# Kernel optimization log

Measured on AMD Instinct MI355X. Metric: run time of the kernel, lower is better.

The kernel has to match this reference:

```python
import jax, jax.numpy as jnp
import numpy as np

LN_EPS = 1e-12


def _conv1d(x, w, b, pad):
    # x: (B, Cin, L), w: (Cout, Cin, K) -> (B, Cout, L)
    y = jax.lax.conv_general_dilated(x, w, window_strides=(1,), padding=[(pad, pad)],
                                     dimension_numbers=('NCH', 'OIH', 'NCH'))
    return y + b[None, :, None]


def setup_inputs() -> dict:
    key = jax.random.key(0)
    ks = jax.random.split(key, 6)
    B, L, C, KH = 4, 4096, 768, 7
    return {
        'hidden_states': jax.random.normal(ks[0], (B, L, C), jnp.float32),
        'attention_mask': jnp.ones((B, L), jnp.float32),
        'special_tokens_mask': jnp.zeros((B, L), jnp.float32),
        'ln_w': jnp.ones((C,), jnp.float32),
        'ln_b': jnp.zeros((C,), jnp.float32),
        'off_w': jax.random.normal(ks[1], (KH, C, KH), jnp.float32) * 0.02,
        'off_b': jnp.zeros((KH,), jnp.float32),
        'mod_w': jax.random.normal(ks[2], (KH, C, KH), jnp.float32) * 0.02,
        'mod_b': jnp.zeros((KH,), jnp.float32),
        'reg_w': jax.random.normal(ks[3], (C, C, KH), jnp.float32) * 0.02,
    }


def reference(hidden_states, attention_mask, special_tokens_mask,
              ln_w, ln_b, off_w, off_b, mod_w, mod_b, reg_w):
    B, L, C = hidden_states.shape
    kh = off_w.shape[0]
    pad = kh // 2
    residual = hidden_states

    # input layernorm (biased variance, like torch.nn.LayerNorm)
    mu = hidden_states.mean(-1, keepdims=True)
    var = hidden_states.var(-1, keepdims=True)
    h = (hidden_states - mu) * jax.lax.rsqrt(var + LN_EPS) * ln_w + ln_b

    ht = jnp.swapaxes(h, 1, 2)  # (B, C, L)
    off = _conv1d(ht, off_w, off_b, pad)                    # (B, kh, L) seq-axis offsets
    mod = 2.0 * jax.nn.sigmoid(_conv1d(ht, mod_w, mod_b, pad))  # (B, kh, L)

    # mask special tokens / padding before sampling
    gate = ((1.0 - special_tokens_mask) * attention_mask)[:, None, :]
    xm = ht * gate  # (B, C, L)

    # deformable 1D sampling positions: p - pad + k + off[b,k,p]
    base = (jnp.arange(L, dtype=jnp.float32) - pad)[None, :] + jnp.arange(kh, dtype=jnp.float32)[:, None]  # (kh, L)
    pos = base[None, :, :] + off  # (B, kh, L)
    f = jnp.floor(pos)
    t = pos - f                   # (B, kh, L) frac
    fi = f.astype(jnp.int32)

    def gather(idx):
        # linear-sample tap with zero padding outside [0, L-1]
        inb = ((idx >= 0) & (idx <= L - 1)).astype(xm.dtype)  # (B, kh, L)
        idxc = jnp.clip(idx, 0, L - 1)
        v = jax.vmap(lambda xb, ib: xb[:, ib])(xm, idxc)      # (B, C, kh, L)
        return v * inb[:, None, :, :]

    sample = gather(fi) * (1.0 - t)[:, None] + gather(fi + 1) * t[:, None]  # (B, C, kh, L)
    sample = sample * mod[:, None]  # modulated

    out = jnp.einsum('ock,bckp->bop', reg_w, sample)  # (B, C, L)
    out = jnp.swapaxes(out, 1, 2) + residual          # (B, L, C)
    return out
```

## Files before the change

### kernel.cpp

```cpp
#include <hip/hip_runtime.h>
#include <math.h>

#define BB 4
#define LL 4096
#define CC 768
#define KHH 7
#define PADK 3
#define ROWS (BB*LL)
#define NKP  (BB*KHH*LL)
#define GK   (KHH*CC)
#define NT   (GK/64)
#define NKC  (GK/8)

typedef unsigned short ushort8 __attribute__((ext_vector_type(8)));
typedef short short8 __attribute__((ext_vector_type(8)));
typedef float f32x4 __attribute__((ext_vector_type(4)));

__device__ __forceinline__ float bf2f(unsigned short u) {
    return __uint_as_float(((unsigned)u) << 16);
}
__device__ __forceinline__ unsigned short f2bf(float x) {
    unsigned u = __float_as_uint(x);
    return (unsigned short)((u + 0x7FFFu + ((u >> 16) & 1u)) >> 16);
}

__global__ __launch_bounds__(256) void k_ln(const float* __restrict__ x,
        const float* __restrict__ mask, const float* __restrict__ special,
        const float* __restrict__ lnw, const float* __restrict__ lnb,
        unsigned short* __restrict__ hb, float* __restrict__ gate) {
    int row = blockIdx.x;
    const float* xr = x + (size_t)row * CC;
    float s = 0.f, q = 0.f;
    for (int i = threadIdx.x; i < CC; i += 256) { float v = xr[i]; s += v; q += v * v; }
    for (int o = 32; o; o >>= 1) { s += __shfl_xor(s, o); q += __shfl_xor(q, o); }
    __shared__ float ss[4], sq[4];
    int wid = threadIdx.x >> 6;
    if ((threadIdx.x & 63) == 0) { ss[wid] = s; sq[wid] = q; }
    __syncthreads();
    s = ss[0] + ss[1] + ss[2] + ss[3];
    q = sq[0] + sq[1] + sq[2] + sq[3];
    float mu  = s * (1.f / CC);
    float var = fmaxf(q * (1.f / CC) - mu * mu, 0.f);
    float rstd = rsqrtf(var + 1e-12f);
    unsigned short* hr = hb + (size_t)row * CC;
    for (int i = threadIdx.x; i < CC; i += 256)
        hr[i] = f2bf((xr[i] - mu) * rstd * lnw[i] + lnb[i]);
    if (threadIdx.x == 0) gate[row] = (1.f - special[row]) * mask[row];
}

__global__ __launch_bounds__(256) void k_wbt(const float* __restrict__ rw,
                                             unsigned short* __restrict__ wbt) {
    __shared__ float s[GK];
    int o = blockIdx.x;
    for (int i = threadIdx.x; i < GK; i += 256) s[i] = rw[(size_t)o * GK + i];
    __syncthreads();
    for (int kc = threadIdx.x; kc < NKC; kc += 256) {
        int k = kc / 96;
        int c0 = (kc - k * 96) * 8;
        ushort8 r;
#pragma unroll
        for (int e = 0; e < 8; ++e) r[e] = f2bf(s[(c0 + e) * KHH + k]);
        *(ushort8*)(wbt + ((size_t)kc * CC + o) * 8) = r;
    }
}

__global__ __launch_bounds__(256) void k_wcb(const float* __restrict__ ow, const float* __restrict__ mw,
                                             unsigned short* __restrict__ wcb) {
    int i = blockIdx.x;
    for (int c = threadIdx.x; c < CC; c += 256) {
        float v = 0.f;
        if (i < 49)      v = ow[(size_t)(i / 7) * (CC * KHH) + (size_t)c * KHH + (i % 7)];
        else if (i < 98) { int j = i - 49; v = mw[(size_t)(j / 7) * (CC * KHH) + (size_t)c * KHH + (j % 7)]; }
        wcb[(size_t)i * CC + c] = f2bf(v);
    }
}

__global__ __launch_bounds__(256) void k_dg2(const unsigned short* __restrict__ A,
        const unsigned short* __restrict__ Bm, float* __restrict__ d) {
    __shared__ __align__(16) char As[128 * 128];
    __shared__ __align__(16) char Bs[128 * 128];
    int r0 = blockIdx.x * 128;
    int t = threadIdx.x;
    int lane = t & 63, w = t >> 6;
    int wr = w >> 1, wc = w & 1;
    f32x4 acc[4][4];
#pragma unroll
    for (int m = 0; m < 4; ++m)
#pragma unroll
        for (int n = 0; n < 4; ++n) acc[m][n] = (f32x4){0.f, 0.f, 0.f, 0.f};
    int lr = lane & 15;
    int lkb0 = (lane >> 4) * 16;
    for (int kk = 0; kk < CC; kk += 64) {
#pragma unroll
        for (int s = 0; s < 4; ++s) {
            int byteoff = (s * 256 + t) * 16;
            int row = byteoff >> 7;
            int colb = byteoff & 127;
            int sw = (row * 128 + colb) ^ ((row & 7) << 4);
            *(ushort8*)(As + sw) = *(const ushort8*)(A + (size_t)(r0 + row) * CC + kk + (colb >> 1));
            *(ushort8*)(Bs + sw) = *(const ushort8*)(Bm + (size_t)row * CC + kk + (colb >> 1));
        }
        __syncthreads();
#pragma unroll
        for (int ks = 0; ks < 2; ++ks) {
            short8 av[4], bv[4];
            int lkb = lkb0 + ks * 64;
#pragma unroll
            for (int m = 0; m < 4; ++m) {
                int ar = wr * 64 + m * 16 + lr;
                av[m] = *(const short8*)(As + ((ar * 128 + lkb) ^ ((ar & 7) << 4)));
            }
#pragma unroll
            for (int n = 0; n < 4; ++n) {
                int br = wc * 64 + n * 16 + lr;
                bv[n] = *(const short8*)(Bs + ((br * 128 + lkb) ^ ((br & 7) << 4)));
            }
#pragma unroll
            for (int m = 0; m < 4; ++m)
#pragma unroll
                for (int n = 0; n < 4; ++n)
                    acc[m][n] = __builtin_amdgcn_mfma_f32_16x16x32_bf16(av[m], bv[n], acc[m][n], 0, 0, 0);
        }
        __syncthreads();
    }
    int lr4 = (lane >> 4) * 4, lc = lane & 15;
#pragma unroll
    for (int m = 0; m < 4; ++m) {
        int gr = r0 + wr * 64 + m * 16 + lr4;
#pragma unroll
        for (int n = 0; n < 4; ++n) {
            int gc = wc * 64 + n * 16 + lc;
#pragma unroll
            for (int j = 0; j < 4; ++j)
                d[(size_t)(gr + j) * 128 + gc] = acc[m][n][j];
        }
    }
}

__global__ __launch_bounds__(256) void k_off(const float* __restrict__ d,
        const float* __restrict__ offb, const float* __restrict__ modb,
        const float* __restrict__ gate,
        int* __restrict__ idx0, int* __restrict__ idx1,
        float* __restrict__ w0a, float* __restrict__ w1a) {
    int flat = blockIdx.x * 256 + threadIdx.x;
    if (flat >= NKP) return;
    int p = flat & (LL - 1);
    int k = (flat >> 12) % KHH;
    int b = flat / (KHH * LL);
    float offa = offb[k], moda = modb[k];
#pragma unroll
    for (int j = 0; j < KHH; ++j) {
        int q = p + j - PADK;
        if (q >= 0 && q < LL) {
            const float* dr = d + (size_t)(b * LL + q) * 128;
            offa += dr[k * 7 + j];
            moda += dr[49 + k * 7 + j];
        }
    }
    float modv = 2.f / (1.f + expf(-moda));
    float pos = (float)(p - PADK + k) + offa;
    pos = fminf(fmaxf(pos, -1.0e9f), 1.0e9f);
    float f = floorf(pos);
    float tf = pos - f;
    int i0 = (int)f;
    int i1 = i0 + 1;
    float in0 = (i0 >= 0 && i0 < LL) ? 1.f : 0.f;
    float in1 = (i1 >= 0 && i1 < LL) ? 1.f : 0.f;
    int c0 = min(max(i0, 0), LL - 1);
    int c1 = min(max(i1, 0), LL - 1);
    float g0 = gate[b * LL + c0] * in0;
    float g1 = gate[b * LL + c1] * in1;
    w0a[flat] = modv * (1.f - tf) * g0;
    w1a[flat] = modv * tf * g1;
    idx0[flat] = c0;
    idx1[flat] = c1;
}


#define STEPOFF 49152
#define KSOFF   24576

#define LOADB(Q, KS, D0, D1, D2, D3, D4, D5) do { \
    const unsigned short* _q = (Q) + (KS) * KSOFF; \
    D0 = *(const short8*)(_q); \
    D1 = *(const short8*)(_q + 128); \
    D2 = *(const short8*)(_q + 256); \
    D3 = *(const short8*)(_q + 384); \
    D4 = *(const short8*)(_q + 512); \
    D5 = *(const short8*)(_q + 640); \
} while (0)

#define MFMA_ROW(AV, M, B0, B1, B2, B3, B4, B5) \
    acc[M][0] = __builtin_amdgcn_mfma_f32_16x16x32_bf16(AV, B0, acc[M][0], 0, 0, 0); \
    acc[M][1] = __builtin_amdgcn_mfma_f32_16x16x32_bf16(AV, B1, acc[M][1], 0, 0, 0); \
    acc[M][2] = __builtin_amdgcn_mfma_f32_16x16x32_bf16(AV, B2, acc[M][2], 0, 0, 0); \
    acc[M][3] = __builtin_amdgcn_mfma_f32_16x16x32_bf16(AV, B3, acc[M][3], 0, 0, 0); \
    acc[M][4] = __builtin_amdgcn_mfma_f32_16x16x32_bf16(AV, B4, acc[M][4], 0, 0, 0); \
    acc[M][5] = __builtin_amdgcn_mfma_f32_16x16x32_bf16(AV, B5, acc[M][5], 0, 0, 0);

#define COMPUTE_KS(ASB, KS, B0, B1, B2, B3, B4, B5) do { \
    __builtin_amdgcn_s_setprio(1); \
    int _lkb = ke0 * 2 + (KS) * 64; \
    short8 _av0, _av1, _av2, _av3; \
    { int ar = wr * 64 + 0 * 16 + lr; _av0 = *(const short8*)((ASB) + ar * 128 + (_lkb ^ ((ar & 7) << 4))); } \
    { int ar = wr * 64 + 1 * 16 + lr; _av1 = *(const short8*)((ASB) + ar * 128 + (_lkb ^ ((ar & 7) << 4))); } \
    { int ar = wr * 64 + 2 * 16 + lr; _av2 = *(const short8*)((ASB) + ar * 128 + (_lkb ^ ((ar & 7) << 4))); } \
    { int ar = wr * 64 + 3 * 16 + lr; _av3 = *(const short8*)((ASB) + ar * 128 + (_lkb ^ ((ar & 7) << 4))); } \
    MFMA_ROW(_av0, 0, B0, B1, B2, B3, B4, B5) \
    MFMA_ROW(_av1, 1, B0, B1, B2, B3, B4, B5) \
    MFMA_ROW(_av2, 2, B0, B1, B2, B3, B4, B5) \
    MFMA_ROW(_av3, 3, B0, B1, B2, B3, B4, B5) \
    __builtin_amdgcn_s_setprio(0); \
} while (0)

__global__ __launch_bounds__(512, 2) void k_fgemm(const unsigned short* __restrict__ hb,
        const unsigned short* __restrict__ Wbt,
        const int* __restrict__ idx0, const int* __restrict__ idx1,
        const float* __restrict__ w0a, const float* __restrict__ w1a,
        const float* __restrict__ resid, float* __restrict__ out) {
    __shared__ __align__(16) char As[2][128 * 128];

    int bid = blockIdx.x;
    int nhalf = (bid & 7) >> 2;
    int rowtile = (bid >> 3) * 4 + (bid & 3);
    int r0 = rowtile * 128;
    int o0 = nhalf * 384;
    int b = r0 >> 12;
    int p0 = r0 & (LL - 1);
    int pbase = ((b * KHH) << 12) + p0;
    const unsigned short* hbB = hb + (size_t)b * LL * CC;

    int t = threadIdx.x;
    int lane = t & 63, w = t >> 6;
    int wr = w >> 2, wc = w & 3;
    int lr = lane & 15;
    int ke0 = (lane >> 4) * 8;

    const unsigned short* pB = Wbt + ((size_t)(lane >> 4) * CC + o0 + wc * 96 + lr) * 8;

    int arow = t >> 2, aseg = t & 3;
    int acolb = aseg * 32;
    int aswz0 = arow * 128 + (acolb ^ ((arow & 7) << 4));
    int aswz1 = arow * 128 + ((acolb + 16) ^ ((arow & 7) << 4));

    f32x4 acc[4][6];
#pragma unroll
    for (int m = 0; m < 4; ++m)
#pragma unroll
        for (int n = 0; n < 6; ++n) acc[m][n] = (f32x4){0.f, 0.f, 0.f, 0.f};

    int g0 = 0, g1 = 0;
    float wa = 0.f, wbv = 0.f;
    int cur_tap = -1;

    ushort8 la0, la1, la2, la3;
    short8 S0_0, S0_1, S0_2, S0_3, S0_4, S0_5;
    short8 S1_0, S1_1, S1_2, S1_3, S1_4, S1_5;
    short8 S2_0, S2_1, S2_2, S2_3, S2_4, S2_5;

    auto loadA = [&](int tap, int c0) {
        if (tap != cur_tap) {
            int pf = pbase + (tap << 12) + arow;
            g0 = idx0[pf]; g1 = idx1[pf];
            wa = w0a[pf];  wbv = w1a[pf];
            cur_tap = tap;
        }
        const unsigned short* s0 = hbB + (size_t)g0 * CC + c0 + aseg * 16;
        const unsigned short* s1 = hbB + (size_t)g1 * CC + c0 + aseg * 16;
        la0 = *(const ushort8*)(s0);
        la1 = *(const ushort8*)(s0 + 8);
        la2 = *(const ushort8*)(s1);
        la3 = *(const ushort8*)(s1 + 8);
    };

    auto writeA = [&](char* Asb) {
        ushort8 ra, rb;
#pragma unroll
        for (int e = 0; e < 8; ++e) ra[e] = f2bf(fmaf(wa, bf2f(la0[e]), wbv * bf2f(la2[e])));
#pragma unroll
        for (int e = 0; e < 8; ++e) rb[e] = f2bf(fmaf(wa, bf2f(la1[e]), wbv * bf2f(la3[e])));
        *(ushort8*)(Asb + aswz0) = ra;
        *(ushort8*)(Asb + aswz1) = rb;
    };

    loadA(0, 0);
    LOADB(pB, 0, S0_0, S0_1, S0_2, S0_3, S0_4, S0_5);
    LOADB(pB, 1, S1_0, S1_1, S1_2, S1_3, S1_4, S1_5);
    writeA(As[0]);
    __syncthreads();

    int tap_c = 0, c0_c = 0;
    for (int sp = 0; sp < NT; sp += 2) {
        {
            int s = sp;
            int tap_n = tap_c, c0_n = c0_c + 64;
            if (c0_n == CC) { c0_n = 0; ++tap_n; }
            bool more = (s + 1 < NT);
            const unsigned short* pN = pB + STEPOFF;
            if (more) {
                LOADB(pN, 0, S2_0, S2_1, S2_2, S2_3, S2_4, S2_5);
                loadA(tap_n, c0_n);
            }
            __builtin_amdgcn_sched_barrier(0);
            COMPUTE_KS(As[0], 0, S0_0, S0_1, S0_2, S0_3, S0_4, S0_5);
            COMPUTE_KS(As[0], 1, S1_0, S1_1, S1_2, S1_3, S1_4, S1_5);
            __builtin_amdgcn_sched_barrier(0);
            if (more) {
                LOADB(pN, 1, S1_0, S1_1, S1_2, S1_3, S1_4, S1_5);
                writeA(As[1]);
            }
            __syncthreads();
            pB = pN;
            tap_c = tap_n; c0_c = c0_n;
        }
        {
            int s = sp + 1;
            if (s >= NT) break;
            int tap_n = tap_c, c0_n = c0_c + 64;
            if (c0_n == CC) { c0_n = 0; ++tap_n; }
            bool more = (s + 1 < NT);
            const unsigned short* pN = pB + STEPOFF;
            if (more) {
                LOADB(pN, 0, S0_0, S0_1, S0_2, S0_3, S0_4, S0_5);
                loadA(tap_n, c0_n);
            }
            __builtin_amdgcn_sched_barrier(0);
            COMPUTE_KS(As[1], 0, S2_0, S2_1, S2_2, S2_3, S2_4, S2_5);
            COMPUTE_KS(As[1], 1, S1_0, S1_1, S1_2, S1_3, S1_4, S1_5);
            __builtin_amdgcn_sched_barrier(0);
            if (more) {
                LOADB(pN, 1, S1_0, S1_1, S1_2, S1_3, S1_4, S1_5);
                writeA(As[0]);
            }
            __syncthreads();
            pB = pN;
            tap_c = tap_n; c0_c = c0_n;
        }
    }

    int lr4 = (lane >> 4) * 4, lc = lane & 15;
#pragma unroll
    for (int m = 0; m < 4; ++m) {
        int gr = r0 + wr * 64 + m * 16 + lr4;
#pragma unroll
        for (int n = 0; n < 6; ++n) {
            int gc = o0 + wc * 96 + n * 16 + lc;
#pragma unroll
            for (int j = 0; j < 4; ++j) {
                size_t idx = (size_t)(gr + j) * CC + gc;
                out[idx] = acc[m][n][j] + resid[idx];
            }
        }
    }
}

extern "C" void kernel_launch(void* const* d_in, const int* in_sizes, int n_in,
                              void* d_out, int out_size, void* d_ws, size_t ws_size,
                              hipStream_t stream) {
    const float* x   = (const float*)d_in[0];
    const float* am  = (const float*)d_in[1];
    const float* stm = (const float*)d_in[2];
    const float* lnw = (const float*)d_in[3];
    const float* lnb = (const float*)d_in[4];
    const float* ow  = (const float*)d_in[5];
    const float* ob  = (const float*)d_in[6];
    const float* mw  = (const float*)d_in[7];
    const float* mb  = (const float*)d_in[8];
    const float* rw  = (const float*)d_in[9];
    float* out = (float*)d_out;

    char* ws = (char*)d_ws;
    size_t off = 0;
    auto carve = [&](size_t bytes) -> char* {
        char* p = ws + off;
        off += (bytes + 255) & ~(size_t)255;
        return p;
    };
    unsigned short* hb  = (unsigned short*)carve((size_t)ROWS * CC * 2);
    unsigned short* wbt = (unsigned short*)carve((size_t)NKC * CC * 8 * 2);
    unsigned short* wcb = (unsigned short*)carve((size_t)128 * CC * 2);
    float* d    = (float*)carve((size_t)ROWS * 128 * 4);
    float* gate = (float*)carve((size_t)ROWS * 4);
    int*   i0   = (int*)carve((size_t)NKP * 4);
    int*   i1   = (int*)carve((size_t)NKP * 4);
    float* w0   = (float*)carve((size_t)NKP * 4);
    float* w1   = (float*)carve((size_t)NKP * 4);

    k_ln<<<ROWS, 256, 0, stream>>>(x, am, stm, lnw, lnb, hb, gate);
    k_wbt<<<CC, 256, 0, stream>>>(rw, wbt);
    k_wcb<<<128, 256, 0, stream>>>(ow, mw, wcb);
    k_dg2<<<ROWS / 128, 256, 0, stream>>>(hb, wcb, d);
    k_off<<<NKP / 256, 256, 0, stream>>>(d, ob, mb, gate, i0, i1, w0, w1);
    k_fgemm<<<256, 512, 0, stream>>>(hb, wbt, i0, i1, w0, w1, x, out);
}
```

Before: 210.3 us.

## Retile fused gather-GEMM to 128x192 tiles with 4 waves and 512 blocks

Changes the fused deformable-gather GEMM from 128x384 output tiles with 8 waves (2x4) to 128x192 tiles with 4 waves, each wave covering all 128 rows and 48 columns. The grid doubles to 512 blocks of 256 threads, and each thread now gathers and blends 32 channels per step instead of 16. The goal is more blocks per GPU for better load balance and occupancy, and less B-register pressure per wave. The cost is that each gathered A tile is reused across fewer output columns, so the gather and blend work is redone twice as often per output.

```diff
diff --git a/kernel.cpp b/kernel.cpp
--- a/kernel.cpp
+++ b/kernel.cpp
@@ -180,40 +180,42 @@
 #define STEPOFF 49152
 #define KSOFF   24576
 
-#define LOADB(Q, KS, D0, D1, D2, D3, D4, D5) do { \
+#define LOADB3(Q, KS, D0, D1, D2) do { \
     const unsigned short* _q = (Q) + (KS) * KSOFF; \
     D0 = *(const short8*)(_q); \
     D1 = *(const short8*)(_q + 128); \
     D2 = *(const short8*)(_q + 256); \
-    D3 = *(const short8*)(_q + 384); \
-    D4 = *(const short8*)(_q + 512); \
-    D5 = *(const short8*)(_q + 640); \
 } while (0)
 
-#define MFMA_ROW(AV, M, B0, B1, B2, B3, B4, B5) \
+#define MFMA_ROW3(AV, M, B0, B1, B2) \
     acc[M][0] = __builtin_amdgcn_mfma_f32_16x16x32_bf16(AV, B0, acc[M][0], 0, 0, 0); \
     acc[M][1] = __builtin_amdgcn_mfma_f32_16x16x32_bf16(AV, B1, acc[M][1], 0, 0, 0); \
-    acc[M][2] = __builtin_amdgcn_mfma_f32_16x16x32_bf16(AV, B2, acc[M][2], 0, 0, 0); \
-    acc[M][3] = __builtin_amdgcn_mfma_f32_16x16x32_bf16(AV, B3, acc[M][3], 0, 0, 0); \
-    acc[M][4] = __builtin_amdgcn_mfma_f32_16x16x32_bf16(AV, B4, acc[M][4], 0, 0, 0); \
-    acc[M][5] = __builtin_amdgcn_mfma_f32_16x16x32_bf16(AV, B5, acc[M][5], 0, 0, 0);
-
-#define COMPUTE_KS(ASB, KS, B0, B1, B2, B3, B4, B5) do { \
+    acc[M][2] = __builtin_amdgcn_mfma_f32_16x16x32_bf16(AV, B2, acc[M][2], 0, 0, 0);
+
+#define COMPUTE_KS3(ASB, KS, B0, B1, B2) do { \
     __builtin_amdgcn_s_setprio(1); \
     int _lkb = ke0 * 2 + (KS) * 64; \
-    short8 _av0, _av1, _av2, _av3; \
-    { int ar = wr * 64 + 0 * 16 + lr; _av0 = *(const short8*)((ASB) + ar * 128 + (_lkb ^ ((ar & 7) << 4))); } \
-    { int ar = wr * 64 + 1 * 16 + lr; _av1 = *(const short8*)((ASB) + ar * 128 + (_lkb ^ ((ar & 7) << 4))); } \
-    { int ar = wr * 64 + 2 * 16 + lr; _av2 = *(const short8*)((ASB) + ar * 128 + (_lkb ^ ((ar & 7) << 4))); } \
-    { int ar = wr * 64 + 3 * 16 + lr; _av3 = *(const short8*)((ASB) + ar * 128 + (_lkb ^ ((ar & 7) << 4))); } \
-    MFMA_ROW(_av0, 0, B0, B1, B2, B3, B4, B5) \
-    MFMA_ROW(_av1, 1, B0, B1, B2, B3, B4, B5) \
-    MFMA_ROW(_av2, 2, B0, B1, B2, B3, B4, B5) \
-    MFMA_ROW(_av3, 3, B0, B1, B2, B3, B4, B5) \
+    short8 _av0, _av1, _av2, _av3, _av4, _av5, _av6, _av7; \
+    { int ar = 0 * 16 + lr; _av0 = *(const short8*)((ASB) + ar * 128 + (_lkb ^ ((ar & 7) << 4))); } \
+    { int ar = 1 * 16 + lr; _av1 = *(const short8*)((ASB) + ar * 128 + (_lkb ^ ((ar & 7) << 4))); } \
+    { int ar = 2 * 16 + lr; _av2 = *(const short8*)((ASB) + ar * 128 + (_lkb ^ ((ar & 7) << 4))); } \
+    { int ar = 3 * 16 + lr; _av3 = *(const short8*)((ASB) + ar * 128 + (_lkb ^ ((ar & 7) << 4))); } \
+    MFMA_ROW3(_av0, 0, B0, B1, B2) \
+    MFMA_ROW3(_av1, 1, B0, B1, B2) \
+    MFMA_ROW3(_av2, 2, B0, B1, B2) \
+    MFMA_ROW3(_av3, 3, B0, B1, B2) \
+    { int ar = 4 * 16 + lr; _av4 = *(const short8*)((ASB) + ar * 128 + (_lkb ^ ((ar & 7) << 4))); } \
+    { int ar = 5 * 16 + lr; _av5 = *(const short8*)((ASB) + ar * 128 + (_lkb ^ ((ar & 7) << 4))); } \
+    { int ar = 6 * 16 + lr; _av6 = *(const short8*)((ASB) + ar * 128 + (_lkb ^ ((ar & 7) << 4))); } \
+    { int ar = 7 * 16 + lr; _av7 = *(const short8*)((ASB) + ar * 128 + (_lkb ^ ((ar & 7) << 4))); } \
+    MFMA_ROW3(_av4, 4, B0, B1, B2) \
+    MFMA_ROW3(_av5, 5, B0, B1, B2) \
+    MFMA_ROW3(_av6, 6, B0, B1, B2) \
+    MFMA_ROW3(_av7, 7, B0, B1, B2) \
     __builtin_amdgcn_s_setprio(0); \
 } while (0)
 
-__global__ __launch_bounds__(512, 2) void k_fgemm(const unsigned short* __restrict__ hb,
+__global__ __launch_bounds__(256, 2) void k_fgemm(const unsigned short* __restrict__ hb,
         const unsigned short* __restrict__ Wbt,
         const int* __restrict__ idx0, const int* __restrict__ idx1,
         const float* __restrict__ w0a, const float* __restrict__ w1a,
@@ -221,42 +223,44 @@
     __shared__ __align__(16) char As[2][128 * 128];
 
     int bid = blockIdx.x;
-    int nhalf = (bid & 7) >> 2;
-    int rowtile = (bid >> 3) * 4 + (bid & 3);
+    int nq = (bid & 7) >> 1;
+    int rowtile = (bid >> 3) * 2 + (bid & 1);
     int r0 = rowtile * 128;
-    int o0 = nhalf * 384;
+    int o0 = nq * 192;
     int b = r0 >> 12;
     int p0 = r0 & (LL - 1);
     int pbase = ((b * KHH) << 12) + p0;
     const unsigned short* hbB = hb + (size_t)b * LL * CC;
 
     int t = threadIdx.x;
-    int lane = t & 63, w = t >> 6;
-    int wr = w >> 2, wc = w & 3;
+    int lane = t & 63, wc = t >> 6;
     int lr = lane & 15;
     int ke0 = (lane >> 4) * 8;
 
-    const unsigned short* pB = Wbt + ((size_t)(lane >> 4) * CC + o0 + wc * 96 + lr) * 8;
-
-    int arow = t >> 2, aseg = t & 3;
-    int acolb = aseg * 32;
-    int aswz0 = arow * 128 + (acolb ^ ((arow & 7) << 4));
-    int aswz1 = arow * 128 + ((acolb + 16) ^ ((arow & 7) << 4));
-
-    f32x4 acc[4][6];
-#pragma unroll
-    for (int m = 0; m < 4; ++m)
-#pragma unroll
-        for (int n = 0; n < 6; ++n) acc[m][n] = (f32x4){0.f, 0.f, 0.f, 0.f};
+    const unsigned short* pB = Wbt + ((size_t)(lane >> 4) * CC + o0 + wc * 48 + lr) * 8;
+
+    int arow = t >> 1, aseg = t & 1;
+    int abase = arow * 128;
+    int axor = (arow & 7) << 4;
+    int asw0 = abase + ((aseg * 64 +  0) ^ axor);
+    int asw1 = abase + ((aseg * 64 + 16) ^ axor);
+    int asw2 = abase + ((aseg * 64 + 32) ^ axor);
+    int asw3 = abase + ((aseg * 64 + 48) ^ axor);
+
+    f32x4 acc[8][3];
+#pragma unroll
+    for (int m = 0; m < 8; ++m)
+#pragma unroll
+        for (int n = 0; n < 3; ++n) acc[m][n] = (f32x4){0.f, 0.f, 0.f, 0.f};
 
     int g0 = 0, g1 = 0;
     float wa = 0.f, wbv = 0.f;
     int cur_tap = -1;
 
-    ushort8 la0, la1, la2, la3;
-    short8 S0_0, S0_1, S0_2, S0_3, S0_4, S0_5;
-    short8 S1_0, S1_1, S1_2, S1_3, S1_4, S1_5;
-    short8 S2_0, S2_1, S2_2, S2_3, S2_4, S2_5;
+    ushort8 la0, la1, la2, la3, la4, la5, la6, la7;
+    short8 S0_0, S0_1, S0_2;
+    short8 S1_0, S1_1, S1_2;
+    short8 S2_0, S2_1, S2_2;
 
     auto loadA = [&](int tap, int c0) {
         if (tap != cur_tap) {
@@ -265,48 +269,57 @@
             wa = w0a[pf];  wbv = w1a[pf];
             cur_tap = tap;
         }
-        const unsigned short* s0 = hbB + (size_t)g0 * CC + c0 + aseg * 16;
-        const unsigned short* s1 = hbB + (size_t)g1 * CC + c0 + aseg * 16;
+        const unsigned short* s0 = hbB + (size_t)g0 * CC + c0 + aseg * 32;
+        const unsigned short* s1 = hbB + (size_t)g1 * CC + c0 + aseg * 32;
         la0 = *(const ushort8*)(s0);
         la1 = *(const ushort8*)(s0 + 8);
-        la2 = *(const ushort8*)(s1);
-        la3 = *(const ushort8*)(s1 + 8);
+        la2 = *(const ushort8*)(s0 + 16);
+        la3 = *(const ushort8*)(s0 + 24);
+        la4 = *(const ushort8*)(s1);
+        la5 = *(const ushort8*)(s1 + 8);
+        la6 = *(const ushort8*)(s1 + 16);
+        la7 = *(const ushort8*)(s1 + 24);
     };
 
     auto writeA = [&](char* Asb) {
-        ushort8 ra, rb;
-#pragma unroll
-        for (int e = 0; e < 8; ++e) ra[e] = f2bf(fmaf(wa, bf2f(la0[e]), wbv * bf2f(la2[e])));
-#pragma unroll
-        for (int e = 0; e < 8; ++e) rb[e] = f2bf(fmaf(wa, bf2f(la1[e]), wbv * bf2f(la3[e])));
-        *(ushort8*)(Asb + aswz0) = ra;
-        *(ushort8*)(Asb + aswz1) = rb;
+        ushort8 ra0, ra1, ra2, ra3;
+#pragma unroll
+        for (int e = 0; e < 8; ++e) ra0[e] = f2bf(fmaf(wa, bf2f(la0[e]), wbv * bf2f(la4[e])));
+#pragma unroll
+        for (int e = 0; e < 8; ++e) ra1[e] = f2bf(fmaf(wa, bf2f(la1[e]), wbv * bf2f(la5[e])));
+#pragma unroll
+        for (int e = 0; e < 8; ++e) ra2[e] = f2bf(fmaf(wa, bf2f(la2[e]), wbv * bf2f(la6[e])));
+#pragma unroll
+        for (int e = 0; e < 8; ++e) ra3[e] = f2bf(fmaf(wa, bf2f(la3[e]), wbv * bf2f(la7[e])));
+        *(ushort8*)(Asb + asw0) = ra0;
+        *(ushort8*)(Asb + asw1) = ra1;
+        *(ushort8*)(Asb + asw2) = ra2;
+        *(ushort8*)(Asb + asw3) = ra3;
     };
 
     loadA(0, 0);
-    LOADB(pB, 0, S0_0, S0_1, S0_2, S0_3, S0_4, S0_5);
-    LOADB(pB, 1, S1_0, S1_1, S1_2, S1_3, S1_4, S1_5);
+    LOADB3(pB, 0, S0_0, S0_1, S0_2);
+    LOADB3(pB, 1, S1_0, S1_1, S1_2);
     writeA(As[0]);
     __syncthreads();
 
     int tap_c = 0, c0_c = 0;
     for (int sp = 0; sp < NT; sp += 2) {
         {
-            int s = sp;
             int tap_n = tap_c, c0_n = c0_c + 64;
             if (c0_n == CC) { c0_n = 0; ++tap_n; }
-            bool more = (s + 1 < NT);
+            bool more = (sp + 1 < NT);
             const unsigned short* pN = pB + STEPOFF;
             if (more) {
-                LOADB(pN, 0, S2_0, S2_1, S2_2, S2_3, S2_4, S2_5);
+                LOADB3(pN, 0, S2_0, S2_1, S2_2);
                 loadA(tap_n, c0_n);
             }
             __builtin_amdgcn_sched_barrier(0);
-            COMPUTE_KS(As[0], 0, S0_0, S0_1, S0_2, S0_3, S0_4, S0_5);
-            COMPUTE_KS(As[0], 1, S1_0, S1_1, S1_2, S1_3, S1_4, S1_5);
+            COMPUTE_KS3(As[0], 0, S0_0, S0_1, S0_2);
+            COMPUTE_KS3(As[0], 1, S1_0, S1_1, S1_2);
             __builtin_amdgcn_sched_barrier(0);
             if (more) {
-                LOADB(pN, 1, S1_0, S1_1, S1_2, S1_3, S1_4, S1_5);
+                LOADB3(pN, 1, S1_0, S1_1, S1_2);
                 writeA(As[1]);
             }
             __syncthreads();
@@ -321,15 +334,15 @@
             bool more = (s + 1 < NT);
             const unsigned short* pN = pB + STEPOFF;
             if (more) {
-                LOADB(pN, 0, S0_0, S0_1, S0_2, S0_3, S0_4, S0_5);
+                LOADB3(pN, 0, S0_0, S0_1, S0_2);
                 loadA(tap_n, c0_n);
             }
             __builtin_amdgcn_sched_barrier(0);
-            COMPUTE_KS(As[1], 0, S2_0, S2_1, S2_2, S2_3, S2_4, S2_5);
-            COMPUTE_KS(As[1], 1, S1_0, S1_1, S1_2, S1_3, S1_4, S1_5);
+            COMPUTE_KS3(As[1], 0, S2_0, S2_1, S2_2);
+            COMPUTE_KS3(As[1], 1, S1_0, S1_1, S1_2);
             __builtin_amdgcn_sched_barrier(0);
             if (more) {
-                LOADB(pN, 1, S1_0, S1_1, S1_2, S1_3, S1_4, S1_5);
+                LOADB3(pN, 1, S1_0, S1_1, S1_2);
                 writeA(As[0]);
             }
             __syncthreads();
@@ -340,11 +353,11 @@
 
     int lr4 = (lane >> 4) * 4, lc = lane & 15;
 #pragma unroll
-    for (int m = 0; m < 4; ++m) {
-        int gr = r0 + wr * 64 + m * 16 + lr4;
-#pragma unroll
-        for (int n = 0; n < 6; ++n) {
-            int gc = o0 + wc * 96 + n * 16 + lc;
+    for (int m = 0; m < 8; ++m) {
+        int gr = r0 + m * 16 + lr4;
+#pragma unroll
+        for (int n = 0; n < 3; ++n) {
+            int gc = o0 + wc * 48 + n * 16 + lc;
 #pragma unroll
             for (int j = 0; j < 4; ++j) {
                 size_t idx = (size_t)(gr + j) * CC + gc;
@@ -391,5 +404,5 @@
     k_wcb<<<128, 256, 0, stream>>>(ow, mw, wcb);
     k_dg2<<<ROWS / 128, 256, 0, stream>>>(hb, wcb, d);
     k_off<<<NKP / 256, 256, 0, stream>>>(d, ob, mb, gate, i0, i1, w0, w1);
-    k_fgemm<<<256, 512, 0, stream>>>(hb, wbt, i0, i1, w0, w1, x, out);
-}
+    k_fgemm<<<512, 256, 0, stream>>>(hb, wbt, i0, i1, w0, w1, x, out);
+}
```

After: 236.5 us. 12.4% more time.

## Deepen A-gather prefetch to two stages with separate register sets

Applied to the files above, without the earlier changes.

The gathered A-tile loads for the deformable GEMM now use two independent register sets, each advancing by two K-steps, so the global gather for step s+2 is issued while step s computes. The LDS write for the next buffer moves to the start of each half-iteration. __syncthreads is replaced by a custom barrier that waits only on lgkmcnt, leaving global loads in flight across it. This hides gather latency better at the cost of more live registers, which may spill under the 512x2 launch bounds.

```diff
diff --git a/kernel.cpp b/kernel.cpp
--- a/kernel.cpp
+++ b/kernel.cpp
@@ -213,6 +213,12 @@
     __builtin_amdgcn_s_setprio(0); \
 } while (0)
 
+#define BAR() do { \
+    asm volatile("s_waitcnt lgkmcnt(0)" ::: "memory"); \
+    __builtin_amdgcn_s_barrier(); \
+    __builtin_amdgcn_sched_barrier(0); \
+} while (0)
+
 __global__ __launch_bounds__(512, 2) void k_fgemm(const unsigned short* __restrict__ hb,
         const unsigned short* __restrict__ Wbt,
         const int* __restrict__ idx0, const int* __restrict__ idx1,
@@ -249,92 +255,103 @@
 #pragma unroll
         for (int n = 0; n < 6; ++n) acc[m][n] = (f32x4){0.f, 0.f, 0.f, 0.f};
 
-    int g0 = 0, g1 = 0;
-    float wa = 0.f, wbv = 0.f;
-    int cur_tap = -1;
-
-    ushort8 la0, la1, la2, la3;
+    int tap0 = 0, c00 = 0, g0_0 = 0, g1_0 = 0;
+    float wa0 = 0.f, wb0 = 0.f;
+    ushort8 la0_0, la1_0, la2_0, la3_0;
+    int tap1 = 0, c01 = 0, g0_1 = 0, g1_1 = 0;
+    float wa1 = 0.f, wb1 = 0.f;
+    ushort8 la0_1, la1_1, la2_1, la3_1;
+
     short8 S0_0, S0_1, S0_2, S0_3, S0_4, S0_5;
     short8 S1_0, S1_1, S1_2, S1_3, S1_4, S1_5;
     short8 S2_0, S2_1, S2_2, S2_3, S2_4, S2_5;
 
-    auto loadA = [&](int tap, int c0) {
-        if (tap != cur_tap) {
-            int pf = pbase + (tap << 12) + arow;
-            g0 = idx0[pf]; g1 = idx1[pf];
-            wa = w0a[pf];  wbv = w1a[pf];
-            cur_tap = tap;
-        }
-        const unsigned short* s0 = hbB + (size_t)g0 * CC + c0 + aseg * 16;
-        const unsigned short* s1 = hbB + (size_t)g1 * CC + c0 + aseg * 16;
-        la0 = *(const ushort8*)(s0);
-        la1 = *(const ushort8*)(s0 + 8);
-        la2 = *(const ushort8*)(s1);
-        la3 = *(const ushort8*)(s1 + 8);
-    };
-
-    auto writeA = [&](char* Asb) {
+    auto loadIdx0 = [&]() {
+        int pf = pbase + (tap0 << 12) + arow;
+        g0_0 = idx0[pf]; g1_0 = idx1[pf]; wa0 = w0a[pf]; wb0 = w1a[pf];
+    };
+    auto loadIdx1 = [&]() {
+        int pf = pbase + (tap1 << 12) + arow;
+        g0_1 = idx0[pf]; g1_1 = idx1[pf]; wa1 = w0a[pf]; wb1 = w1a[pf];
+    };
+    auto gatherRaw0 = [&]() {
+        const unsigned short* s0 = hbB + (size_t)g0_0 * CC + c00 + aseg * 16;
+        const unsigned short* s1 = hbB + (size_t)g1_0 * CC + c00 + aseg * 16;
+        la0_0 = *(const ushort8*)(s0);
+        la1_0 = *(const ushort8*)(s0 + 8);
+        la2_0 = *(const ushort8*)(s1);
+        la3_0 = *(const ushort8*)(s1 + 8);
+    };
+    auto gatherRaw1 = [&]() {
+        const unsigned short* s0 = hbB + (size_t)g0_1 * CC + c01 + aseg * 16;
+        const unsigned short* s1 = hbB + (size_t)g1_1 * CC + c01 + aseg * 16;
+        la0_1 = *(const ushort8*)(s0);
+        la1_1 = *(const ushort8*)(s0 + 8);
+        la2_1 = *(const ushort8*)(s1);
+        la3_1 = *(const ushort8*)(s1 + 8);
+    };
+    auto gatherAdv0 = [&]() {
+        c00 += 128;
+        if (c00 >= CC) { c00 -= CC; ++tap0; loadIdx0(); }
+        gatherRaw0();
+    };
+    auto gatherAdv1 = [&]() {
+        c01 += 128;
+        if (c01 >= CC) { c01 -= CC; ++tap1; loadIdx1(); }
+        gatherRaw1();
+    };
+    auto writeA0 = [&](char* Asb) {
         ushort8 ra, rb;
 #pragma unroll
-        for (int e = 0; e < 8; ++e) ra[e] = f2bf(fmaf(wa, bf2f(la0[e]), wbv * bf2f(la2[e])));
-#pragma unroll
-        for (int e = 0; e < 8; ++e) rb[e] = f2bf(fmaf(wa, bf2f(la1[e]), wbv * bf2f(la3[e])));
+        for (int e = 0; e < 8; ++e) ra[e] = f2bf(fmaf(wa0, bf2f(la0_0[e]), wb0 * bf2f(la2_0[e])));
+#pragma unroll
+        for (int e = 0; e < 8; ++e) rb[e] = f2bf(fmaf(wa0, bf2f(la1_0[e]), wb0 * bf2f(la3_0[e])));
         *(ushort8*)(Asb + aswz0) = ra;
         *(ushort8*)(Asb + aswz1) = rb;
     };
-
-    loadA(0, 0);
+    auto writeA1 = [&](char* Asb) {
+        ushort8 ra, rb;
+#pragma unroll
+        for (int e = 0; e < 8; ++e) ra[e] = f2bf(fmaf(wa1, bf2f(la0_1[e]), wb1 * bf2f(la2_1[e])));
+#pragma unroll
+        for (int e = 0; e < 8; ++e) rb[e] = f2bf(fmaf(wa1, bf2f(la1_1[e]), wb1 * bf2f(la3_1[e])));
+        *(ushort8*)(Asb + aswz0) = ra;
+        *(ushort8*)(Asb + aswz1) = rb;
+    };
+
+    tap0 = 0; c00 = 0; loadIdx0(); gatherRaw0();
+    tap1 = 0; c01 = 64; loadIdx1(); gatherRaw1();
     LOADB(pB, 0, S0_0, S0_1, S0_2, S0_3, S0_4, S0_5);
     LOADB(pB, 1, S1_0, S1_1, S1_2, S1_3, S1_4, S1_5);
-    writeA(As[0]);
-    __syncthreads();
-
-    int tap_c = 0, c0_c = 0;
+    writeA0(As[0]);
+    BAR();
+
     for (int sp = 0; sp < NT; sp += 2) {
         {
-            int s = sp;
-            int tap_n = tap_c, c0_n = c0_c + 64;
-            if (c0_n == CC) { c0_n = 0; ++tap_n; }
-            bool more = (s + 1 < NT);
+            bool gmore = (sp + 2 < NT);
             const unsigned short* pN = pB + STEPOFF;
-            if (more) {
-                LOADB(pN, 0, S2_0, S2_1, S2_2, S2_3, S2_4, S2_5);
-                loadA(tap_n, c0_n);
-            }
+            writeA1(As[1]);
             __builtin_amdgcn_sched_barrier(0);
+            if (gmore) gatherAdv0();
+            LOADB(pN, 0, S2_0, S2_1, S2_2, S2_3, S2_4, S2_5);
             COMPUTE_KS(As[0], 0, S0_0, S0_1, S0_2, S0_3, S0_4, S0_5);
             COMPUTE_KS(As[0], 1, S1_0, S1_1, S1_2, S1_3, S1_4, S1_5);
+            LOADB(pN, 1, S1_0, S1_1, S1_2, S1_3, S1_4, S1_5);
+            BAR();
+        }
+        {
+            bool wmore = (sp + 2 < NT);
+            bool gmore = (sp + 3 < NT);
+            const unsigned short* pN2 = pB + 2 * STEPOFF;
+            if (wmore) writeA0(As[0]);
             __builtin_amdgcn_sched_barrier(0);
-            if (more) {
-                LOADB(pN, 1, S1_0, S1_1, S1_2, S1_3, S1_4, S1_5);
-                writeA(As[1]);
-            }
-            __syncthreads();
-            pB = pN;
-            tap_c = tap_n; c0_c = c0_n;
-        }
-        {
-            int s = sp + 1;
-            if (s >= NT) break;
-            int tap_n = tap_c, c0_n = c0_c + 64;
-            if (c0_n == CC) { c0_n = 0; ++tap_n; }
-            bool more = (s + 1 < NT);
-            const unsigned short* pN = pB + STEPOFF;
-            if (more) {
-                LOADB(pN, 0, S0_0, S0_1, S0_2, S0_3, S0_4, S0_5);
-                loadA(tap_n, c0_n);
-            }
-            __builtin_amdgcn_sched_barrier(0);
+            if (gmore) gatherAdv1();
+            if (wmore) LOADB(pN2, 0, S0_0, S0_1, S0_2, S0_3, S0_4, S0_5);
             COMPUTE_KS(As[1], 0, S2_0, S2_1, S2_2, S2_3, S2_4, S2_5);
             COMPUTE_KS(As[1], 1, S1_0, S1_1, S1_2, S1_3, S1_4, S1_5);
-            __builtin_amdgcn_sched_barrier(0);
-            if (more) {
-                LOADB(pN, 1, S1_0, S1_1, S1_2, S1_3, S1_4, S1_5);
-                writeA(As[0]);
-            }
-            __syncthreads();
-            pB = pN;
-            tap_c = tap_n; c0_c = c0_n;
+            if (wmore) LOADB(pN2, 1, S1_0, S1_1, S1_2, S1_3, S1_4, S1_5);
+            BAR();
+            pB = pN2;
         }
     }
 
```

Measured after the change: 262.7 us. 24.9% more time.
